# Optimization experiments

Hardware: AMD Instinct MI355X
Metric: run time of the kernel (lower is better)

Reference implementation:

```python
import jax, jax.numpy as jnp
import numpy as np

REFSIZE = 1024  # init kwarg refsize -> self.N
EPS = float(np.finfo(np.float32).eps)


def interp1d(x, y, xnew):
    """Batched linear interpolation, faithful to Interp1d.forward.
    x, y: (D, N) with x sorted along last dim; xnew: (D, P). Returns (D, P)."""
    # torch.searchsorted default (right=False) == numpy/jnp side='left'
    ind = jax.vmap(jnp.searchsorted)(x, xnew) - 1
    ind = jnp.clip(ind, 0, x.shape[1] - 2)
    slopes = (y[:, 1:] - y[:, :-1]) / (EPS + (x[:, 1:] - x[:, :-1]))
    x_sel = jnp.take_along_axis(x, ind, axis=1)
    y_sel = jnp.take_along_axis(y, ind, axis=1)
    s_sel = jnp.take_along_axis(slopes, ind, axis=1)
    return y_sel + s_sel * (xnew - x_sel)


def setup_inputs() -> dict:
    key = jax.random.key(0)
    k1, k2 = jax.random.split(key)
    l, n = 2048, 4096
    x1 = jax.random.uniform(k1, (l, n), dtype=jnp.float32)  # points on [0,1)
    w = jax.random.uniform(k2, (l, n), dtype=jnp.float32)
    x1_weights = w / jnp.sum(w, axis=-1, keepdims=True)  # row-normalized masses
    return {"x1": x1, "x1_weights": x1_weights}


def reference(x1, x1_weights):
    l, n = x1.shape
    N = REFSIZE
    ref = jnp.linspace(0.0, 1.0, N + 1, dtype=jnp.float32)[:-1]  # (N,)

    # empirical_cdf: sort samples, cumsum weights
    order = jnp.argsort(x1, axis=-1)
    xs = jnp.take_along_axis(x1, order, axis=-1)          # (l, n) sorted samples
    ys = jnp.cumsum(jnp.take_along_axis(x1_weights, order, axis=-1), axis=-1)  # CDF

    # emb
    alpha = (jnp.sum(x1 * x1_weights, axis=-1) / jnp.sum(x1_weights, axis=-1) - 0.5)[:, None]
    xnew = jnp.broadcast_to(jnp.linspace(-1.0, 2.0, 3 * N, dtype=jnp.float32)[None, :], (l, 3 * N))
    int_x = jnp.floor(xnew)
    rest_x = xnew - int_x
    ecdf = int_x + interp1d(xs, ys, rest_x)               # (l, 3N) extended CDF

    x_grid = jnp.broadcast_to(ref[None, :], (l, N))
    embedd = interp1d(ecdf, xnew, x_grid - alpha) - x_grid  # inverse-CDF embedding

    # circular cost
    a = jnp.abs(embedd)
    m = jnp.minimum(a, 1.0 - a)
    return jnp.sqrt(jnp.mean(jnp.sum(m * m, axis=-1)) + 1e-8)
```

## Files before the change

kernel.cpp:

```cpp
#include <hip/hip_runtime.h>
#include <math.h>

#define L    2048
#define NCOL 4096
#define NG   1024
#define N3   3072
#define T    512
#define NW   8
#define EPT  8
#define NB   2048
#define FEPS 1.1920929e-07f

typedef unsigned long long u64;
typedef unsigned short u16;
typedef unsigned int u32;

__device__ __forceinline__ int lower_bound_f(const float* a, int lo, int hi, float v) {
  while (lo < hi) {
    int mid = (lo + hi) >> 1;
    if (a[mid] < v) lo = mid + 1; else hi = mid;
  }
  return lo;
}

__device__ __forceinline__ int bucket_of_bits(unsigned xb) {
  float f = __uint_as_float(xb);
  int b = (int)(f * (float)NB);
  return b > NB - 1 ? NB - 1 : b;
}

__global__ __launch_bounds__(T, 8) void lcot_rows(const float* __restrict__ X,
                                                  const float* __restrict__ W,
                                                  float* __restrict__ rowsum) {
  extern __shared__ char smem[];
  u64*   pairs = (u64*)smem;
  float* xs    = (float*)smem;
  float* ys    = (float*)(smem + 16384);
  float* ecdf  = (float*)(smem + 16384);
  u16*   cnt16 = (u16*)(smem + 32768);
  u32*   cntw  = (u32*)(smem + 32768);
  u16*   lut2  = (u16*)(smem + 36872);

  __shared__ float redA[NW], redB[NW], fwt[NW];
  __shared__ int   iwt[NW];
  __shared__ float s_alpha;

  const int tid  = threadIdx.x;
  const int lane = tid & 63;
  const int wave = tid >> 6;
  const int row  = blockIdx.x;
  const float* xr = X + (size_t)row * NCOL;
  const float* wr = W + (size_t)row * NCOL;

  for (int i = tid; i < 1025; i += T) cntw[i] = 0u;

  u64 key[EPT];
  float sxw = 0.f, sw = 0.f;
  const float4* xr4 = (const float4*)xr;
  const float4* wr4 = (const float4*)wr;
#pragma unroll
  for (int c = 0; c < 2; ++c) {
    float4 xv = xr4[tid * 2 + c];
    float4 ww = wr4[tid * 2 + c];
    sxw += xv.x * ww.x + xv.y * ww.y + xv.z * ww.z + xv.w * ww.w;
    sw  += ww.x + ww.y + ww.z + ww.w;
    int b = 8 * tid + 4 * c;
    key[4*c+0] = ((u64)__float_as_uint(xv.x) << 32) | (unsigned)(b + 0);
    key[4*c+1] = ((u64)__float_as_uint(xv.y) << 32) | (unsigned)(b + 1);
    key[4*c+2] = ((u64)__float_as_uint(xv.z) << 32) | (unsigned)(b + 2);
    key[4*c+3] = ((u64)__float_as_uint(xv.w) << 32) | (unsigned)(b + 3);
  }
#pragma unroll
  for (int off = 32; off > 0; off >>= 1) {
    sxw += __shfl_down(sxw, off);
    sw  += __shfl_down(sw, off);
  }
  if (lane == 0) { redA[wave] = sxw; redB[wave] = sw; }
  __syncthreads();

  int ord[EPT];
#pragma unroll
  for (int e = 0; e < EPT; ++e) {
    int b = bucket_of_bits((unsigned)(key[e] >> 32));
    u32 inc = (b & 1) ? 65536u : 1u;
    u32 ret = atomicAdd(&cntw[b >> 1], inc);
    ord[e] = (b & 1) ? (int)(ret >> 16) : (int)(ret & 0xffffu);
  }
  __syncthreads();
  if (tid == 0) {
    float a = 0.f, b = 0.f;
#pragma unroll
    for (int i = 0; i < NW; ++i) { a += redA[i]; b += redB[i]; }
    s_alpha = a / b - 0.5f;
  }

  u32 cv0 = cntw[2 * tid], cv1 = cntw[2 * tid + 1];
  int c0 = (int)(cv0 & 0xffffu), c1 = (int)(cv0 >> 16);
  int c2 = (int)(cv1 & 0xffffu), c3 = (int)(cv1 >> 16);
  int runi = c0 + c1 + c2 + c3;
  int toti = runi, prei = runi;
#pragma unroll
  for (int off = 1; off < 64; off <<= 1) {
    int v = __shfl_up(prei, off);
    if (lane >= off) prei += v;
  }
  if (lane == 63) iwt[wave] = prei;
  __syncthreads();
  int wpre = 0;
#pragma unroll
  for (int w2 = 0; w2 < NW; ++w2) wpre += (w2 < wave) ? iwt[w2] : 0;
  int acc = wpre + prei - toti;
  {
    int b0 = acc; acc += c0;
    int b1 = acc; acc += c1;
    int b2 = acc; acc += c2;
    int b3 = acc; acc += c3;
    cntw[2 * tid]     = (u32)b0 | ((u32)b1 << 16);
    cntw[2 * tid + 1] = (u32)b2 | ((u32)b3 << 16);
  }
  if (tid == T - 1) cnt16[NB] = (u16)acc;
  __syncthreads();

#pragma unroll
  for (int e = 0; e < EPT; ++e) {
    int b = bucket_of_bits((unsigned)(key[e] >> 32));
    pairs[(int)cnt16[b] + ord[e]] = key[e];
  }
  __syncthreads();

#pragma unroll
  for (int bb = 0; bb < 4; ++bb) {
    int b  = 4 * tid + bb;
    int lo = (int)cnt16[b], hi = (int)cnt16[b + 1];
    for (int i = lo + 1; i < hi; ++i) {
      u64 v = pairs[i];
      int j = i - 1;
      while (j >= lo && pairs[j] > v) { pairs[j + 1] = pairs[j]; --j; }
      pairs[j + 1] = v;
    }
  }
  __syncthreads();

  u64 q[EPT];
  {
    const ulonglong2* pr2 = (const ulonglong2*)pairs + 4 * tid;
#pragma unroll
    for (int c = 0; c < 4; ++c) { ulonglong2 v = pr2[c]; q[2*c] = v.x; q[2*c+1] = v.y; }
  }
  float wg[EPT];
#pragma unroll
  for (int e = 0; e < EPT; ++e) wg[e] = wr[(u32)(q[e] & 0xffffffffu)];
  __syncthreads();

  {
    float4 xa0, xa1;
    xa0.x = __uint_as_float((u32)(q[0] >> 32));
    xa0.y = __uint_as_float((u32)(q[1] >> 32));
    xa0.z = __uint_as_float((u32)(q[2] >> 32));
    xa0.w = __uint_as_float((u32)(q[3] >> 32));
    xa1.x = __uint_as_float((u32)(q[4] >> 32));
    xa1.y = __uint_as_float((u32)(q[5] >> 32));
    xa1.z = __uint_as_float((u32)(q[6] >> 32));
    xa1.w = __uint_as_float((u32)(q[7] >> 32));
    ((float4*)xs)[2 * tid]     = xa0;
    ((float4*)xs)[2 * tid + 1] = xa1;
  }
  float lw[EPT];
  float runf = 0.f;
#pragma unroll
  for (int c = 0; c < EPT; ++c) { runf += wg[c]; lw[c] = runf; }
  float totf = runf, pref = runf;
#pragma unroll
  for (int off = 1; off < 64; off <<= 1) {
    float v = __shfl_up(pref, off);
    if (lane >= off) pref += v;
  }
  if (lane == 63) fwt[wave] = pref;
  __syncthreads();
  float wpf = 0.f;
#pragma unroll
  for (int w2 = 0; w2 < NW; ++w2) wpf += (w2 < wave) ? fwt[w2] : 0.f;
  float basef = wpf + pref - totf;
  {
    ((float4*)ys)[2 * tid]     = make_float4(basef + lw[0], basef + lw[1],
                                             basef + lw[2], basef + lw[3]);
    ((float4*)ys)[2 * tid + 1] = make_float4(basef + lw[4], basef + lw[5],
                                             basef + lw[6], basef + lw[7]);
  }
  __syncthreads();

  float ev[N3 / T];
#pragma unroll
  for (int s = 0; s < N3 / T; ++s) {
    int j = tid + s * T;
    float xnew = -1.0f + (3.0f * (float)j) / 3071.0f;
    float ix = floorf(xnew);
    float rest = xnew - ix;
    int k = (int)(rest * (float)NB);
    k = k > NB - 1 ? NB - 1 : k;
    int lo = lower_bound_f(xs, (int)cnt16[k], (int)cnt16[k + 1], rest);
    int ind = lo - 1;
    ind = ind < 0 ? 0 : (ind > NCOL - 2 ? NCOL - 2 : ind);
    float x0 = xs[ind], x1v = xs[ind + 1];
    float y0 = ys[ind], y1v = ys[ind + 1];
    float slope = (y1v - y0) * __builtin_amdgcn_rcpf(FEPS + (x1v - x0));
    ev[s] = ix + (y0 + slope * (rest - x0));
  }
  __syncthreads();

#pragma unroll
  for (int s = 0; s < N3 / T; ++s) ecdf[tid + s * T] = ev[s];
  __syncthreads();

  if (tid < 257) {
    float v = -1.0f + 3.0f * (float)tid * (1.0f / 256.0f);
    lut2[tid] = (u16)lower_bound_f(ecdf, 0, N3, v);
  }
  __syncthreads();

  float alpha = s_alpha;
  float accf = 0.f;
#pragma unroll
  for (int s = 0; s < NG / T; ++s) {
    int kq = tid + s * T;
    float xg = (float)kq / 1024.0f;
    float q2 = xg - alpha;
    int k2 = (int)floorf((q2 + 1.0f) * (256.0f / 3.0f));
    k2 = k2 < 0 ? 0 : (k2 > 255 ? 255 : k2);
    int blo = k2 > 0 ? k2 - 1 : 0;
    int bhi = k2 < 254 ? k2 + 2 : 256;
    int lo = lower_bound_f(ecdf, (int)lut2[blo], (int)lut2[bhi], q2);
    int ind = lo - 1;
    ind = ind < 0 ? 0 : (ind > N3 - 2 ? N3 - 2 : ind);
    float e0 = ecdf[ind], e1 = ecdf[ind + 1];
    float y0 = -1.0f + (3.0f * (float)ind) / 3071.0f;
    float y1 = -1.0f + (3.0f * (float)(ind + 1)) / 3071.0f;
    float slope = (y1 - y0) * __builtin_amdgcn_rcpf(FEPS + (e1 - e0));
    float emb = y0 + slope * (q2 - e0) - xg;
    float a = fabsf(emb);
    float m = fminf(a, 1.0f - a);
    accf += m * m;
  }
#pragma unroll
  for (int off = 32; off > 0; off >>= 1) accf += __shfl_down(accf, off);
  if (lane == 0) redA[wave] = accf;
  __syncthreads();
  if (tid == 0) {
    float s = 0.f;
#pragma unroll
    for (int i = 0; i < NW; ++i) s += redA[i];
    rowsum[row] = s;
  }
}

__global__ __launch_bounds__(256) void lcot_final(const float* __restrict__ rowsum,
                                                  float* __restrict__ out) {
  __shared__ float red[4];
  int t = threadIdx.x;
  float s = 0.f;
  for (int i = t; i < L; i += 256) s += rowsum[i];
#pragma unroll
  for (int off = 32; off > 0; off >>= 1) s += __shfl_down(s, off);
  if ((t & 63) == 0) red[t >> 6] = s;
  __syncthreads();
  if (t == 0) {
    float tot = red[0] + red[1] + red[2] + red[3];
    out[0] = sqrtf(tot / (float)L + 1e-8f);
  }
}

extern "C" void kernel_launch(void* const* d_in, const int* in_sizes, int n_in,
                              void* d_out, int out_size, void* d_ws, size_t ws_size,
                              hipStream_t stream) {
  const float* X = (const float*)d_in[0];
  const float* W = (const float*)d_in[1];
  float* rowsum = (float*)d_ws;
  size_t shbytes = 32768 + 4104 + 520;
  hipLaunchKernelGGL(lcot_rows, dim3(L), dim3(T), shbytes, stream, X, W, rowsum);
  hipLaunchKernelGGL(lcot_final, dim3(1), dim3(256), 0, stream,
                     (const float*)rowsum, (float*)d_out);
}
```

Measured before the change: 178.5 us.

## Replace in-bucket insertion sort with rank-by-counting scatter and unrolled bucket search

Replaces the serial per-bucket insertion sort with a per-element rank computation: each thread counts smaller keys in its bucket (first four unrolled, tail looped) and scatters x and weight directly to their sorted positions. This also removes the gather of weights from global memory by original index, replacing it with a coalesced float4 load and a scatter into a swizzled shared array. The bucket lookup for interpolation becomes an unrolled four-compare linear scan with a rare tail loop instead of a binary search. The intent is to cut divergent serial sorting and random global loads, at the cost of more shared-memory reads per element and reliance on bucket sizes mostly being small.

```diff
diff --git a/kernel.cpp b/kernel.cpp
--- a/kernel.cpp
+++ b/kernel.cpp
@@ -29,13 +29,15 @@
   return b > NB - 1 ? NB - 1 : b;
 }
 
+__device__ __forceinline__ int swz(int i) { return i ^ ((i >> 5) & 7); }
+
 __global__ __launch_bounds__(T, 8) void lcot_rows(const float* __restrict__ X,
                                                   const float* __restrict__ W,
                                                   float* __restrict__ rowsum) {
   extern __shared__ char smem[];
   u64*   pairs = (u64*)smem;
   float* xs    = (float*)smem;
-  float* ys    = (float*)(smem + 16384);
+  float* wy    = (float*)(smem + 16384);
   float* ecdf  = (float*)(smem + 16384);
   u16*   cnt16 = (u16*)(smem + 32768);
   u32*   cntw  = (u32*)(smem + 32768);
@@ -128,47 +130,56 @@
   }
   __syncthreads();
 
-#pragma unroll
-  for (int bb = 0; bb < 4; ++bb) {
-    int b  = 4 * tid + bb;
+  int dst[EPT]; int tailhi[EPT];
+#pragma unroll
+  for (int e = 0; e < EPT; ++e) {
+    int b = bucket_of_bits((unsigned)(key[e] >> 32));
     int lo = (int)cnt16[b], hi = (int)cnt16[b + 1];
-    for (int i = lo + 1; i < hi; ++i) {
-      u64 v = pairs[i];
-      int j = i - 1;
-      while (j >= lo && pairs[j] > v) { pairs[j + 1] = pairs[j]; --j; }
-      pairs[j + 1] = v;
+    int hm1 = hi - 1;
+    u64 k = key[e];
+    u64 p0 = pairs[lo];
+    u64 p1 = pairs[lo + 1 < hm1 ? lo + 1 : hm1];
+    u64 p2 = pairs[lo + 2 < hm1 ? lo + 2 : hm1];
+    u64 p3 = pairs[lo + 3 < hm1 ? lo + 3 : hm1];
+    int n = hi - lo;
+    int r = (int)(p0 < k) + (int)(n > 1 && p1 < k)
+          + (int)(n > 2 && p2 < k) + (int)(n > 3 && p3 < k);
+    dst[e] = lo + r;
+    tailhi[e] = (n > 4) ? hi : 0;
+  }
+#pragma unroll
+  for (int e = 0; e < EPT; ++e) {
+    if (tailhi[e]) {
+      int b = bucket_of_bits((unsigned)(key[e] >> 32));
+      int lo = (int)cnt16[b];
+      u64 k = key[e];
+      int r = 0;
+      for (int j2 = lo + 4; j2 < tailhi[e]; ++j2) r += (int)(pairs[j2] < k);
+      dst[e] += r;
     }
   }
-  __syncthreads();
-
-  u64 q[EPT];
+
+  float4 wv0 = wr4[tid * 2], wv1 = wr4[tid * 2 + 1];
+  __syncthreads();
+
   {
-    const ulonglong2* pr2 = (const ulonglong2*)pairs + 4 * tid;
-#pragma unroll
-    for (int c = 0; c < 4; ++c) { ulonglong2 v = pr2[c]; q[2*c] = v.x; q[2*c+1] = v.y; }
-  }
-  float wg[EPT];
-#pragma unroll
-  for (int e = 0; e < EPT; ++e) wg[e] = wr[(u32)(q[e] & 0xffffffffu)];
-  __syncthreads();
-
-  {
-    float4 xa0, xa1;
-    xa0.x = __uint_as_float((u32)(q[0] >> 32));
-    xa0.y = __uint_as_float((u32)(q[1] >> 32));
-    xa0.z = __uint_as_float((u32)(q[2] >> 32));
-    xa0.w = __uint_as_float((u32)(q[3] >> 32));
-    xa1.x = __uint_as_float((u32)(q[4] >> 32));
-    xa1.y = __uint_as_float((u32)(q[5] >> 32));
-    xa1.z = __uint_as_float((u32)(q[6] >> 32));
-    xa1.w = __uint_as_float((u32)(q[7] >> 32));
-    ((float4*)xs)[2 * tid]     = xa0;
-    ((float4*)xs)[2 * tid + 1] = xa1;
-  }
+    float wv[EPT] = {wv0.x, wv0.y, wv0.z, wv0.w, wv1.x, wv1.y, wv1.z, wv1.w};
+#pragma unroll
+    for (int e = 0; e < EPT; ++e) {
+      int d = dst[e];
+      xs[d]       = __uint_as_float((u32)(key[e] >> 32));
+      wy[swz(d)]  = wv[e];
+    }
+  }
+  __syncthreads();
+
   float lw[EPT];
   float runf = 0.f;
 #pragma unroll
-  for (int c = 0; c < EPT; ++c) { runf += wg[c]; lw[c] = runf; }
+  for (int c = 0; c < EPT; ++c) {
+    float wv = wy[swz(8 * tid + c)];
+    runf += wv; lw[c] = runf;
+  }
   float totf = runf, pref = runf;
 #pragma unroll
   for (int off = 1; off < 64; off <<= 1) {
@@ -181,28 +192,52 @@
 #pragma unroll
   for (int w2 = 0; w2 < NW; ++w2) wpf += (w2 < wave) ? fwt[w2] : 0.f;
   float basef = wpf + pref - totf;
-  {
-    ((float4*)ys)[2 * tid]     = make_float4(basef + lw[0], basef + lw[1],
-                                             basef + lw[2], basef + lw[3]);
-    ((float4*)ys)[2 * tid + 1] = make_float4(basef + lw[4], basef + lw[5],
-                                             basef + lw[6], basef + lw[7]);
-  }
+#pragma unroll
+  for (int c = 0; c < EPT; ++c) wy[swz(8 * tid + c)] = basef + lw[c];
   __syncthreads();
 
   float ev[N3 / T];
+  int lb1[N3 / T], lo1[N3 / T], n1[N3 / T];
+#pragma unroll
+  for (int s = 0; s < N3 / T; ++s) {
+    int j = tid + s * T;
+    float xnew = -1.0f + (3.0f * (float)j) / 3071.0f;
+    float rest = xnew - floorf(xnew);
+    int k = (int)(rest * (float)NB);
+    k = k > NB - 1 ? NB - 1 : k;
+    int lo = (int)cnt16[k], hi = (int)cnt16[k + 1];
+    int n = hi - lo;
+    float a0 = xs[lo + 0 < NCOL - 1 ? lo + 0 : NCOL - 1];
+    float a1 = xs[lo + 1 < NCOL - 1 ? lo + 1 : NCOL - 1];
+    float a2 = xs[lo + 2 < NCOL - 1 ? lo + 2 : NCOL - 1];
+    float a3 = xs[lo + 3 < NCOL - 1 ? lo + 3 : NCOL - 1];
+    int c = (int)(n > 0 && a0 < rest) + (int)(n > 1 && a1 < rest)
+          + (int)(n > 2 && a2 < rest) + (int)(n > 3 && a3 < rest);
+    lb1[s] = lo + c;
+    lo1[s] = lo; n1[s] = n;
+  }
+#pragma unroll
+  for (int s = 0; s < N3 / T; ++s) {
+    if (n1[s] > 4 && lb1[s] == lo1[s] + 4) {
+      int j = tid + s * T;
+      float xnew = -1.0f + (3.0f * (float)j) / 3071.0f;
+      float rest = xnew - floorf(xnew);
+      int hi = lo1[s] + n1[s];
+      int p = lo1[s] + 4;
+      while (p < hi && xs[p] < rest) ++p;
+      lb1[s] = p;
+    }
+  }
 #pragma unroll
   for (int s = 0; s < N3 / T; ++s) {
     int j = tid + s * T;
     float xnew = -1.0f + (3.0f * (float)j) / 3071.0f;
     float ix = floorf(xnew);
     float rest = xnew - ix;
-    int k = (int)(rest * (float)NB);
-    k = k > NB - 1 ? NB - 1 : k;
-    int lo = lower_bound_f(xs, (int)cnt16[k], (int)cnt16[k + 1], rest);
-    int ind = lo - 1;
+    int ind = lb1[s] - 1;
     ind = ind < 0 ? 0 : (ind > NCOL - 2 ? NCOL - 2 : ind);
     float x0 = xs[ind], x1v = xs[ind + 1];
-    float y0 = ys[ind], y1v = ys[ind + 1];
+    float y0 = wy[swz(ind)], y1v = wy[swz(ind + 1)];
     float slope = (y1v - y0) * __builtin_amdgcn_rcpf(FEPS + (x1v - x0));
     ev[s] = ix + (y0 + slope * (rest - x0));
   }
```

After: 224.7 us. 25.9% more time.

## Coalesce sorted-pair reads and weight gathers via strided layout with swizzled LDS

Applied to the files above, without the earlier changes.

Threads now read sorted pairs with a stride of T instead of a contiguous 8-element chunk, so the global gathers of weights by original index become more coalesced across a wavefront. The weights are staged through a swizzled shared-memory buffer so each thread can still compute its contiguous prefix sum, and the swizzle is meant to reduce bank conflicts. The CDF values stay in the swizzled layout and are read through the same swizzle during interpolation. Separately, the bucket id is packed alongside the atomic offset so the bucket computation is not repeated during the scatter. The cost is an extra barrier and scalar (non-vector) LDS stores.

```diff
diff --git a/kernel.cpp b/kernel.cpp
--- a/kernel.cpp
+++ b/kernel.cpp
@@ -29,13 +29,15 @@
   return b > NB - 1 ? NB - 1 : b;
 }
 
+__device__ __forceinline__ int swz(int i) { return i ^ ((i >> 5) & 7); }
+
 __global__ __launch_bounds__(T, 8) void lcot_rows(const float* __restrict__ X,
                                                   const float* __restrict__ W,
                                                   float* __restrict__ rowsum) {
   extern __shared__ char smem[];
   u64*   pairs = (u64*)smem;
   float* xs    = (float*)smem;
-  float* ys    = (float*)(smem + 16384);
+  float* wy    = (float*)(smem + 16384);
   float* ecdf  = (float*)(smem + 16384);
   u16*   cnt16 = (u16*)(smem + 32768);
   u32*   cntw  = (u32*)(smem + 32768);
@@ -78,13 +80,14 @@
   if (lane == 0) { redA[wave] = sxw; redB[wave] = sw; }
   __syncthreads();
 
-  int ord[EPT];
+  u32 bo[EPT];
 #pragma unroll
   for (int e = 0; e < EPT; ++e) {
     int b = bucket_of_bits((unsigned)(key[e] >> 32));
     u32 inc = (b & 1) ? 65536u : 1u;
     u32 ret = atomicAdd(&cntw[b >> 1], inc);
-    ord[e] = (b & 1) ? (int)(ret >> 16) : (int)(ret & 0xffffu);
+    u32 o = (b & 1) ? (ret >> 16) : (ret & 0xffffu);
+    bo[e] = ((u32)b << 16) | (o & 0xffffu);
   }
   __syncthreads();
   if (tid == 0) {
@@ -123,8 +126,9 @@
 
 #pragma unroll
   for (int e = 0; e < EPT; ++e) {
-    int b = bucket_of_bits((unsigned)(key[e] >> 32));
-    pairs[(int)cnt16[b] + ord[e]] = key[e];
+    int b = (int)(bo[e] >> 16);
+    int o = (int)(bo[e] & 0xffffu);
+    pairs[(int)cnt16[b] + o] = key[e];
   }
   __syncthreads();
 
@@ -142,33 +146,28 @@
   __syncthreads();
 
   u64 q[EPT];
-  {
-    const ulonglong2* pr2 = (const ulonglong2*)pairs + 4 * tid;
-#pragma unroll
-    for (int c = 0; c < 4; ++c) { ulonglong2 v = pr2[c]; q[2*c] = v.x; q[2*c+1] = v.y; }
-  }
+#pragma unroll
+  for (int m = 0; m < EPT; ++m) q[m] = pairs[tid + m * T];
   float wg[EPT];
 #pragma unroll
-  for (int e = 0; e < EPT; ++e) wg[e] = wr[(u32)(q[e] & 0xffffffffu)];
-  __syncthreads();
-
-  {
-    float4 xa0, xa1;
-    xa0.x = __uint_as_float((u32)(q[0] >> 32));
-    xa0.y = __uint_as_float((u32)(q[1] >> 32));
-    xa0.z = __uint_as_float((u32)(q[2] >> 32));
-    xa0.w = __uint_as_float((u32)(q[3] >> 32));
-    xa1.x = __uint_as_float((u32)(q[4] >> 32));
-    xa1.y = __uint_as_float((u32)(q[5] >> 32));
-    xa1.z = __uint_as_float((u32)(q[6] >> 32));
-    xa1.w = __uint_as_float((u32)(q[7] >> 32));
-    ((float4*)xs)[2 * tid]     = xa0;
-    ((float4*)xs)[2 * tid + 1] = xa1;
-  }
+  for (int m = 0; m < EPT; ++m) wg[m] = wr[(u32)(q[m] & 0xffffffffu)];
+  __syncthreads();
+
+#pragma unroll
+  for (int m = 0; m < EPT; ++m) {
+    int j = tid + m * T;
+    xs[j]      = __uint_as_float((u32)(q[m] >> 32));
+    wy[swz(j)] = wg[m];
+  }
+  __syncthreads();
+
   float lw[EPT];
   float runf = 0.f;
 #pragma unroll
-  for (int c = 0; c < EPT; ++c) { runf += wg[c]; lw[c] = runf; }
+  for (int c = 0; c < EPT; ++c) {
+    runf += wy[swz(8 * tid + c)];
+    lw[c] = runf;
+  }
   float totf = runf, pref = runf;
 #pragma unroll
   for (int off = 1; off < 64; off <<= 1) {
@@ -181,12 +180,8 @@
 #pragma unroll
   for (int w2 = 0; w2 < NW; ++w2) wpf += (w2 < wave) ? fwt[w2] : 0.f;
   float basef = wpf + pref - totf;
-  {
-    ((float4*)ys)[2 * tid]     = make_float4(basef + lw[0], basef + lw[1],
-                                             basef + lw[2], basef + lw[3]);
-    ((float4*)ys)[2 * tid + 1] = make_float4(basef + lw[4], basef + lw[5],
-                                             basef + lw[6], basef + lw[7]);
-  }
+#pragma unroll
+  for (int c = 0; c < EPT; ++c) wy[swz(8 * tid + c)] = basef + lw[c];
   __syncthreads();
 
   float ev[N3 / T];
@@ -202,7 +197,7 @@
     int ind = lo - 1;
     ind = ind < 0 ? 0 : (ind > NCOL - 2 ? NCOL - 2 : ind);
     float x0 = xs[ind], x1v = xs[ind + 1];
-    float y0 = ys[ind], y1v = ys[ind + 1];
+    float y0 = wy[swz(ind)], y1v = wy[swz(ind + 1)];
     float slope = (y1v - y0) * __builtin_amdgcn_rcpf(FEPS + (x1v - x0));
     ev[s] = ix + (y0 + slope * (rest - x0));
   }
```

Measured after the change: 181.9 us. No clear change (+1.9%).
